# Performance work log

Hardware: AMD Instinct MI355X
Metric: run time of the kernel (lower is better)

The kernel has to match this reference:

```python
import jax, jax.numpy as jnp
import numpy as np

B, N, D = 32, 2048, 1024


def setup_inputs() -> dict:
    key = jax.random.key(0)
    k1, k2, k3, k4, k5, k6 = jax.random.split(key, 6)
    encoded = jax.random.normal(k1, (B, N, D), dtype=jnp.float32)
    decoder_state = jax.random.normal(k2, (B, D), dtype=jnp.float32)
    mask = jax.random.randint(k3, (B, N), 0, 2, dtype=jnp.int32)
    scale = 1.0 / np.sqrt(D)
    W1 = jax.random.normal(k4, (D, D), dtype=jnp.float32) * scale  # applied as x @ W1
    W2 = jax.random.normal(k5, (D, D), dtype=jnp.float32) * scale
    vt = jax.random.normal(k6, (D,), dtype=jnp.float32) * scale
    return {"encoded": encoded, "decoder_state": decoder_state, "mask": mask,
            "W1": W1, "W2": W2, "vt": vt}


def reference(encoded, decoder_state, mask, W1, W2, vt):
    temperature = 1.0
    # process_encoded: W1(encoded)  [B, N, D]
    enc = jnp.einsum('bnd,de->bne', encoded, W1)
    # W2(decoder_state)  [B, D] -> broadcast-add over N
    dec = decoder_state @ W2
    # vt(tanh(.)).squeeze(2)  -> logits [B, N]
    u = jnp.einsum('bnd,d->bn', jnp.tanh(enc + dec[:, None, :]), vt)
    # masked log-softmax with temperature over dim=1
    logits = u / temperature + jnp.log(mask.astype(u.dtype) + 1e-45)
    return jax.nn.log_softmax(logits, axis=1)
```

## Files before the change

kernel.cpp:

```cpp
#include <hip/hip_runtime.h>

typedef _Float16 half8 __attribute__((ext_vector_type(8)));
typedef __fp16   pk2   __attribute__((ext_vector_type(2)));
typedef float    f32x4 __attribute__((ext_vector_type(4)));

#define GLOBAL_AS __attribute__((address_space(1)))
#define LDS_AS    __attribute__((address_space(3)))

static constexpr int Bb = 32;
static constexpr int Nn = 2048;
static constexpr int Dd = 1024;
static constexpr int M  = Bb * Nn;

__global__ void prep_w1(const float* __restrict__ W1, _Float16* __restrict__ W1TT) {
    int g = blockIdx.x * 256 + threadIdx.x;
    int tile = g >> 9;
    int u = g & 511;
    int et = tile >> 5, kt = tile & 31;
    int q = u >> 7, e = u & 127;
    int d0 = kt * 32 + q * 8;
    int col = et * 128 + e;
    half8 h;
#pragma unroll
    for (int j = 0; j < 8; ++j)
        h[j] = (_Float16)W1[(size_t)(d0 + j) * Dd + col];
    *(half8*)(W1TT + (size_t)g * 8) = h;
}

__global__ void prep_enc(const float* __restrict__ A, _Float16* __restrict__ A_p) {
    int g = blockIdx.x * 256 + threadIdx.x;
    int tile = g >> 9;
    int v = g & 511;
    int row = v >> 2, kc = v & 3;
    const float* src = A + ((size_t)(tile >> 5) * 128 + row) * Dd
                         + (tile & 31) * 32 + kc * 8;
    f32x4 f0 = *(const f32x4*)src;
    f32x4 f1 = *(const f32x4*)(src + 4);
    half8 h;
    pk2 t;
    t = __builtin_amdgcn_cvt_pkrtz(f0.x, f0.y); h[0] = t[0]; h[1] = t[1];
    t = __builtin_amdgcn_cvt_pkrtz(f0.z, f0.w); h[2] = t[0]; h[3] = t[1];
    t = __builtin_amdgcn_cvt_pkrtz(f1.x, f1.y); h[4] = t[0]; h[5] = t[1];
    t = __builtin_amdgcn_cvt_pkrtz(f1.z, f1.w); h[6] = t[0]; h[7] = t[1];
    *(half8*)(A_p + (size_t)g * 8) = h;
}

__global__ void dec_kernel(const float* __restrict__ ds, const float* __restrict__ W2,
                           float* __restrict__ dec) {
    __shared__ float part[4][64];
    int b = blockIdx.x, ech = blockIdx.y;
    int tid = threadIdx.x;
    int e = ech * 64 + (tid & 63);
    int dc = tid >> 6;
    float acc = 0.f;
#pragma unroll 4
    for (int d = dc * 256; d < dc * 256 + 256; ++d)
        acc += ds[b * Dd + d] * W2[(size_t)d * Dd + e];
    part[dc][tid & 63] = acc;
    __syncthreads();
    if (tid < 64)
        dec[b * Dd + e] = part[0][tid] + part[1][tid] + part[2][tid] + part[3][tid];
}

__global__ __launch_bounds__(256) void gemm_fused_h(
    const _Float16* __restrict__ A_p,
    const _Float16* __restrict__ W1TT,
    const float* __restrict__ dec,
    const float* __restrict__ vt,
    float* __restrict__ u_part)
{
    __shared__ _Float16 As[2][4096];
    __shared__ _Float16 Bs[2][4096];
    __shared__ float usum[2][128];

    const int g = blockIdx.x;
    const int et = (g >> 3) & 7;
    const int mtile = (g & 7) + ((g >> 6) << 3);
    const int tid = threadIdx.x;
    const int lane = tid & 63, wid = tid >> 6;
    const int wm = wid & 1, we = wid >> 1;
    const int q = lane >> 4, l15 = lane & 15;

    f32x4 acc[4][4] = {};

    const int b = mtile >> 4;
    float vtv[4], dcv[4];
#pragma unroll
    for (int nt = 0; nt < 4; ++nt) {
        int e = et * 128 + we * 64 + nt * 16 + l15;
        vtv[nt] = vt[e];
        dcv[nt] = dec[b * Dd + e];
    }
    asm volatile("s_waitcnt vmcnt(0)" ::: "memory");

    const _Float16* abase = A_p + (size_t)mtile * 32 * 4096
                            + ((size_t)(wid * 2) * 64 + lane) * 8;
    const _Float16* bbase = W1TT + (size_t)et * 32 * 4096
                            + ((size_t)(wid * 2) * 64 + lane) * 8;
    _Float16* adst[2] = { &As[0][(wid * 2) * 64 * 8], &As[1][(wid * 2) * 64 * 8] };
    _Float16* bdst[2] = { &Bs[0][(wid * 2) * 64 * 8], &Bs[1][(wid * 2) * 64 * 8] };

    auto issue = [&](int kt) {
        const _Float16* ak = abase + (size_t)kt * 4096;
        const _Float16* bk = bbase + (size_t)kt * 4096;
        const int s = kt & 1;
        __builtin_amdgcn_global_load_lds((const GLOBAL_AS void*)ak,
                                         (LDS_AS void*)adst[s], 16, 0, 0);
        __builtin_amdgcn_global_load_lds((const GLOBAL_AS void*)(ak + 512),
                                         (LDS_AS void*)(adst[s] + 512), 16, 0, 0);
        __builtin_amdgcn_global_load_lds((const GLOBAL_AS void*)bk,
                                         (LDS_AS void*)bdst[s], 16, 0, 0);
        __builtin_amdgcn_global_load_lds((const GLOBAL_AS void*)(bk + 512),
                                         (LDS_AS void*)(bdst[s] + 512), 16, 0, 0);
    };

    issue(0);

#pragma unroll 1
    for (int kt = 0; kt < 32; ++kt) {
        const int s = kt & 1;
        if (kt < 31) {
            issue(kt + 1);
            asm volatile("s_waitcnt vmcnt(4)" ::: "memory");
        } else {
            asm volatile("s_waitcnt vmcnt(0)" ::: "memory");
        }
        asm volatile("s_barrier" ::: "memory");

        half8 af[4], bf[4];
#pragma unroll
        for (int mt = 0; mt < 4; ++mt)
            af[mt] = *(const half8*)&As[s][(wm * 64 + mt * 16 + l15) * 32 + q * 8];
#pragma unroll
        for (int nt = 0; nt < 4; ++nt)
            bf[nt] = *(const half8*)&Bs[s][(q * 128 + we * 64 + nt * 16 + l15) * 8];
#pragma unroll
        for (int mt = 0; mt < 4; ++mt)
#pragma unroll
            for (int nt = 0; nt < 4; ++nt)
                acc[mt][nt] = __builtin_amdgcn_mfma_f32_16x16x32_f16(
                    af[mt], bf[nt], acc[mt][nt], 0, 0, 0);

        asm volatile("s_waitcnt lgkmcnt(0)" ::: "memory");
        asm volatile("s_barrier" ::: "memory");
    }

#pragma unroll
    for (int mt = 0; mt < 4; ++mt) {
#pragma unroll
        for (int r = 0; r < 4; ++r) {
            float s = 0.f;
#pragma unroll
            for (int nt = 0; nt < 4; ++nt) {
                float x = acc[mt][nt][r] + dcv[nt];
                float ex = __expf(2.f * x);
                float th = 1.f - 2.f * __builtin_amdgcn_rcpf(ex + 1.f);
                s += th * vtv[nt];
            }
#pragma unroll
            for (int off = 1; off < 16; off <<= 1) s += __shfl_xor(s, off, 16);
            if (l15 == 0) usum[we][wm * 64 + mt * 16 + q * 4 + r] = s;
        }
    }
    __syncthreads();
    if (tid < 128)
        u_part[(size_t)et * M + (size_t)mtile * 128 + tid] = usum[0][tid] + usum[1][tid];
}

__global__ __launch_bounds__(256) void gemm_fused_f32(
    const float* __restrict__ A, const _Float16* __restrict__ W1TT,
    const float* __restrict__ dec, const float* __restrict__ vt,
    float* __restrict__ u_part)
{
    __shared__ _Float16 As2[4 * 128 * 8];
    __shared__ _Float16 Bs2[512 * 8];
    __shared__ float usum[2][128];

    const int et = blockIdx.x, mtile = blockIdx.y;
    const int tid = threadIdx.x;
    const int lane = tid & 63, wid = tid >> 6;
    const int wm = wid & 1, we = wid >> 1;
    const int q = lane >> 4, l15 = lane & 15;
    f32x4 acc[4][4] = {};

    const int arow = tid >> 1, khalf = tid & 1;
    const float* aptr = A + (size_t)(mtile * 128 + arow) * Dd + khalf * 16;
    const int q0 = khalf * 2;
    const _Float16* bbase = W1TT + (size_t)et * 32 * 4096
                            + ((size_t)(wid * 2) * 64 + lane) * 8;
    _Float16* bdst0 = &Bs2[(wid * 2 + 0) * 64 * 8];
    _Float16* bdst1 = &Bs2[(wid * 2 + 1) * 64 * 8];

#pragma unroll 1
    for (int kt = 0; kt < 32; ++kt) {
        const _Float16* bk = bbase + (size_t)kt * 4096;
        __builtin_amdgcn_global_load_lds((const GLOBAL_AS void*)bk,
                                         (LDS_AS void*)bdst0, 16, 0, 0);
        __builtin_amdgcn_global_load_lds((const GLOBAL_AS void*)(bk + 512),
                                         (LDS_AS void*)bdst1, 16, 0, 0);
        const float4* ap = (const float4*)(aptr + kt * 32);
        float4 f0 = ap[0], f1 = ap[1], f2 = ap[2], f3 = ap[3];
        half8 h0, h1;
        {
            pk2 t;
            t = __builtin_amdgcn_cvt_pkrtz(f0.x, f0.y); h0[0] = t[0]; h0[1] = t[1];
            t = __builtin_amdgcn_cvt_pkrtz(f0.z, f0.w); h0[2] = t[0]; h0[3] = t[1];
            t = __builtin_amdgcn_cvt_pkrtz(f1.x, f1.y); h0[4] = t[0]; h0[5] = t[1];
            t = __builtin_amdgcn_cvt_pkrtz(f1.z, f1.w); h0[6] = t[0]; h0[7] = t[1];
            t = __builtin_amdgcn_cvt_pkrtz(f2.x, f2.y); h1[0] = t[0]; h1[1] = t[1];
            t = __builtin_amdgcn_cvt_pkrtz(f2.z, f2.w); h1[2] = t[0]; h1[3] = t[1];
            t = __builtin_amdgcn_cvt_pkrtz(f3.x, f3.y); h1[4] = t[0]; h1[5] = t[1];
            t = __builtin_amdgcn_cvt_pkrtz(f3.z, f3.w); h1[6] = t[0]; h1[7] = t[1];
        }
        *(half8*)&As2[((q0 + 0) * 128 + arow) * 8] = h0;
        *(half8*)&As2[((q0 + 1) * 128 + arow) * 8] = h1;
        __syncthreads();

        half8 af[4], bf[4];
#pragma unroll
        for (int mt = 0; mt < 4; ++mt)
            af[mt] = *(const half8*)&As2[(q * 128 + wm * 64 + mt * 16 + l15) * 8];
#pragma unroll
        for (int nt = 0; nt < 4; ++nt)
            bf[nt] = *(const half8*)&Bs2[(q * 128 + we * 64 + nt * 16 + l15) * 8];
#pragma unroll
        for (int mt = 0; mt < 4; ++mt)
#pragma unroll
            for (int nt = 0; nt < 4; ++nt)
                acc[mt][nt] = __builtin_amdgcn_mfma_f32_16x16x32_f16(
                    af[mt], bf[nt], acc[mt][nt], 0, 0, 0);
        __syncthreads();
    }

    const int b = mtile >> 4;
    float vtv[4], dcv[4];
#pragma unroll
    for (int nt = 0; nt < 4; ++nt) {
        int e = et * 128 + we * 64 + nt * 16 + l15;
        vtv[nt] = vt[e];
        dcv[nt] = dec[b * Dd + e];
    }
#pragma unroll
    for (int mt = 0; mt < 4; ++mt) {
#pragma unroll
        for (int r = 0; r < 4; ++r) {
            float s = 0.f;
#pragma unroll
            for (int nt = 0; nt < 4; ++nt) {
                float x = acc[mt][nt][r] + dcv[nt];
                float ex = __expf(2.f * x);
                float th = 1.f - 2.f * __builtin_amdgcn_rcpf(ex + 1.f);
                s += th * vtv[nt];
            }
#pragma unroll
            for (int off = 1; off < 16; off <<= 1) s += __shfl_xor(s, off, 16);
            if (l15 == 0) usum[we][wm * 64 + mt * 16 + q * 4 + r] = s;
        }
    }
    __syncthreads();
    if (tid < 128)
        u_part[(size_t)et * M + (size_t)mtile * 128 + tid] = usum[0][tid] + usum[1][tid];
}

__global__ void softmax_k(const float* __restrict__ up, const int* __restrict__ mask,
                          float* __restrict__ out) {
    __shared__ float red[8];
    int b = blockIdx.x, tid = threadIdx.x;
    float l[8];
#pragma unroll
    for (int i = 0; i < 8; ++i) {
        int n = i * 256 + tid;
        float s = up[(size_t)b * Nn + n];
#pragma unroll
        for (int et = 1; et < 8; ++et) s += up[(size_t)et * M + (size_t)b * Nn + n];
        l[i] = s + (mask[b * Nn + n] ? 0.f : -103.278931f);
    }
    float m = l[0];
#pragma unroll
    for (int i = 1; i < 8; ++i) m = fmaxf(m, l[i]);
#pragma unroll
    for (int o = 32; o >= 1; o >>= 1) m = fmaxf(m, __shfl_xor(m, o, 64));
    if ((tid & 63) == 0) red[tid >> 6] = m;
    __syncthreads();
    m = fmaxf(fmaxf(red[0], red[1]), fmaxf(red[2], red[3]));
    float s = 0.f;
#pragma unroll
    for (int i = 0; i < 8; ++i) s += expf(l[i] - m);
#pragma unroll
    for (int o = 32; o >= 1; o >>= 1) s += __shfl_xor(s, o, 64);
    if ((tid & 63) == 0) red[4 + (tid >> 6)] = s;
    __syncthreads();
    float lse = m + logf(red[4] + red[5] + red[6] + red[7]);
#pragma unroll
    for (int i = 0; i < 8; ++i)
        out[(size_t)b * Nn + i * 256 + tid] = l[i] - lse;
}

extern "C" void kernel_launch(void* const* d_in, const int* in_sizes, int n_in,
                              void* d_out, int out_size, void* d_ws, size_t ws_size,
                              hipStream_t stream) {
    const float* encoded = (const float*)d_in[0];
    const float* dstate  = (const float*)d_in[1];
    const int*   mask    = (const int*)d_in[2];
    const float* W1      = (const float*)d_in[3];
    const float* W2      = (const float*)d_in[4];
    const float* vt      = (const float*)d_in[5];
    float* out = (float*)d_out;

    char* ws = (char*)d_ws;
    float*    u_part = (float*)ws;
    float*    dec    = (float*)(ws + (size_t)8 * M * 4);
    _Float16* W1TT   = (_Float16*)(ws + (size_t)8 * M * 4 + (size_t)Bb * Dd * 4);
    _Float16* A_p    = (_Float16*)(ws + (size_t)8 * M * 4 + (size_t)Bb * Dd * 4
                                   + (size_t)Dd * Dd * 2);
    const size_t needed = (size_t)8 * M * 4 + (size_t)Bb * Dd * 4
                        + (size_t)Dd * Dd * 2 + (size_t)M * Dd * 2;

    prep_w1<<<512, 256, 0, stream>>>(W1, W1TT);
    dec_kernel<<<dim3(32, 16), 256, 0, stream>>>(dstate, W2, dec);
    if (ws_size >= needed) {
        prep_enc<<<32768, 256, 0, stream>>>(encoded, A_p);
        gemm_fused_h<<<4096, 256, 0, stream>>>(A_p, W1TT, dec, vt, u_part);
    } else {
        gemm_fused_f32<<<dim3(8, 512), 256, 0, stream>>>(encoded, W1TT, dec, vt, u_part);
    }
    softmax_k<<<32, 256, 0, stream>>>(u_part, mask, out);
}
```

Measured before the change: 596.1 us.

## Replace 128x128 GEMM with 256x256-tile 8-wave kernel using swizzled LDS layout

Replaces the 128x128-tile fused GEMM with a 256x256-tile, 512-thread kernel that uses 128KB of dynamic LDS. It splits each K-step into four MFMA quadrants with staged global-to-LDS prefetches, barriers and s_setprio, and remaps workgroups across XCDs. The prep kernels now write an XOR-swizzled 64-wide K-chunk layout (prep_enc transposes through LDS) to avoid bank conflicts, and u_part drops from 8 to 4 E-partials. The goal is more data reuse per tile and better MFMA utilisation. It also removes the fp32 fallback path that ran when workspace was too small, and the big LDS footprint limits occupancy to one block per CU.

```diff
diff --git a/kernel.cpp b/kernel.cpp
--- a/kernel.cpp
+++ b/kernel.cpp
@@ -12,37 +12,52 @@
 static constexpr int Dd = 1024;
 static constexpr int M  = Bb * Nn;
 
+
 __global__ void prep_w1(const float* __restrict__ W1, _Float16* __restrict__ W1TT) {
     int g = blockIdx.x * 256 + threadIdx.x;
-    int tile = g >> 9;
-    int u = g & 511;
-    int et = tile >> 5, kt = tile & 31;
-    int q = u >> 7, e = u & 127;
-    int d0 = kt * 32 + q * 8;
-    int col = et * 128 + e;
-    half8 h;
+    int chunk = g >> 10;
+    int u = g & 1023;
+    int q = u >> 7, sc = u & 127;
+    int cl = sc ^ (2 * (q & 3));
+    int et = chunk >> 5, t = (chunk >> 1) & 15, h = chunk & 1;
+    int e  = et * 256 + h * 128 + cl;
+    int k0 = t * 64 + q * 8;
+    half8 hh;
 #pragma unroll
     for (int j = 0; j < 8; ++j)
-        h[j] = (_Float16)W1[(size_t)(d0 + j) * Dd + col];
-    *(half8*)(W1TT + (size_t)g * 8) = h;
+        hh[j] = (_Float16)W1[(size_t)(k0 + j) * Dd + e];
+    *(half8*)(W1TT + (size_t)g * 8) = hh;
 }
 
 __global__ void prep_enc(const float* __restrict__ A, _Float16* __restrict__ A_p) {
-    int g = blockIdx.x * 256 + threadIdx.x;
-    int tile = g >> 9;
-    int v = g & 511;
-    int row = v >> 2, kc = v & 3;
-    const float* src = A + ((size_t)(tile >> 5) * 128 + row) * Dd
-                         + (tile & 31) * 32 + kc * 8;
-    f32x4 f0 = *(const f32x4*)src;
-    f32x4 f1 = *(const f32x4*)(src + 4);
-    half8 h;
-    pk2 t;
-    t = __builtin_amdgcn_cvt_pkrtz(f0.x, f0.y); h[0] = t[0]; h[1] = t[1];
-    t = __builtin_amdgcn_cvt_pkrtz(f0.z, f0.w); h[2] = t[0]; h[3] = t[1];
-    t = __builtin_amdgcn_cvt_pkrtz(f1.x, f1.y); h[4] = t[0]; h[5] = t[1];
-    t = __builtin_amdgcn_cvt_pkrtz(f1.z, f1.w); h[6] = t[0]; h[7] = t[1];
-    *(half8*)(A_p + (size_t)g * 8) = h;
+    __shared__ _Float16 T[128 * 64];
+    const int c = blockIdx.x;
+    const int tid = threadIdx.x;
+    const int mtile = c >> 5, t = (c >> 1) & 15, h = c & 1;
+    const int r = tid >> 1, kh = tid & 1;
+    const float* src = A + (size_t)(mtile * 256 + h * 128 + r) * Dd + t * 64 + kh * 32;
+    const int rx = r & 7;
+#pragma unroll
+    for (int i = 0; i < 4; ++i) {
+        f32x4 a  = *(const f32x4*)(src + i * 8);
+        f32x4 b2 = *(const f32x4*)(src + i * 8 + 4);
+        half8 hh; pk2 p;
+        p = __builtin_amdgcn_cvt_pkrtz(a.x, a.y);   hh[0] = p[0]; hh[1] = p[1];
+        p = __builtin_amdgcn_cvt_pkrtz(a.z, a.w);   hh[2] = p[0]; hh[3] = p[1];
+        p = __builtin_amdgcn_cvt_pkrtz(b2.x, b2.y); hh[4] = p[0]; hh[5] = p[1];
+        p = __builtin_amdgcn_cvt_pkrtz(b2.z, b2.w); hh[6] = p[0]; hh[7] = p[1];
+        *(half8*)(T + r * 64 + (((kh * 4 + i) ^ rx) * 8)) = hh;
+    }
+    __syncthreads();
+    const size_t cb = (size_t)c * 8192;
+#pragma unroll
+    for (int i = 0; i < 4; ++i) {
+        int u = i * 256 + tid;
+        int q = u >> 7, sr = u & 127;
+        int lr = sr ^ (2 * (q & 3));
+        half8 hh = *(const half8*)(T + lr * 64 + ((q ^ (lr & 7)) * 8));
+        *(half8*)(A_p + cb + (size_t)u * 8) = hh;
+    }
 }
 
 __global__ void dec_kernel(const float* __restrict__ ds, const float* __restrict__ W2,
@@ -62,204 +77,183 @@
         dec[b * Dd + e] = part[0][tid] + part[1][tid] + part[2][tid] + part[3][tid];
 }
 
-__global__ __launch_bounds__(256) void gemm_fused_h(
-    const _Float16* __restrict__ A_p,
-    const _Float16* __restrict__ W1TT,
-    const float* __restrict__ dec,
-    const float* __restrict__ vt,
-    float* __restrict__ u_part)
-{
-    __shared__ _Float16 As[2][4096];
-    __shared__ _Float16 Bs[2][4096];
-    __shared__ float usum[2][128];
-
-    const int g = blockIdx.x;
-    const int et = (g >> 3) & 7;
-    const int mtile = (g & 7) + ((g >> 6) << 3);
-    const int tid = threadIdx.x;
-    const int lane = tid & 63, wid = tid >> 6;
-    const int wm = wid & 1, we = wid >> 1;
-    const int q = lane >> 4, l15 = lane & 15;
-
-    f32x4 acc[4][4] = {};
-
-    const int b = mtile >> 4;
-    float vtv[4], dcv[4];
-#pragma unroll
-    for (int nt = 0; nt < 4; ++nt) {
-        int e = et * 128 + we * 64 + nt * 16 + l15;
-        vtv[nt] = vt[e];
-        dcv[nt] = dec[b * Dd + e];
-    }
-    asm volatile("s_waitcnt vmcnt(0)" ::: "memory");
-
-    const _Float16* abase = A_p + (size_t)mtile * 32 * 4096
-                            + ((size_t)(wid * 2) * 64 + lane) * 8;
-    const _Float16* bbase = W1TT + (size_t)et * 32 * 4096
-                            + ((size_t)(wid * 2) * 64 + lane) * 8;
-    _Float16* adst[2] = { &As[0][(wid * 2) * 64 * 8], &As[1][(wid * 2) * 64 * 8] };
-    _Float16* bdst[2] = { &Bs[0][(wid * 2) * 64 * 8], &Bs[1][(wid * 2) * 64 * 8] };
-
-    auto issue = [&](int kt) {
-        const _Float16* ak = abase + (size_t)kt * 4096;
-        const _Float16* bk = bbase + (size_t)kt * 4096;
-        const int s = kt & 1;
-        __builtin_amdgcn_global_load_lds((const GLOBAL_AS void*)ak,
-                                         (LDS_AS void*)adst[s], 16, 0, 0);
-        __builtin_amdgcn_global_load_lds((const GLOBAL_AS void*)(ak + 512),
-                                         (LDS_AS void*)(adst[s] + 512), 16, 0, 0);
-        __builtin_amdgcn_global_load_lds((const GLOBAL_AS void*)bk,
-                                         (LDS_AS void*)bdst[s], 16, 0, 0);
-        __builtin_amdgcn_global_load_lds((const GLOBAL_AS void*)(bk + 512),
-                                         (LDS_AS void*)(bdst[s] + 512), 16, 0, 0);
-    };
-
-    issue(0);
-
-#pragma unroll 1
-    for (int kt = 0; kt < 32; ++kt) {
-        const int s = kt & 1;
-        if (kt < 31) {
-            issue(kt + 1);
-            asm volatile("s_waitcnt vmcnt(4)" ::: "memory");
-        } else {
-            asm volatile("s_waitcnt vmcnt(0)" ::: "memory");
-        }
-        asm volatile("s_barrier" ::: "memory");
-
-        half8 af[4], bf[4];
-#pragma unroll
-        for (int mt = 0; mt < 4; ++mt)
-            af[mt] = *(const half8*)&As[s][(wm * 64 + mt * 16 + l15) * 32 + q * 8];
-#pragma unroll
-        for (int nt = 0; nt < 4; ++nt)
-            bf[nt] = *(const half8*)&Bs[s][(q * 128 + we * 64 + nt * 16 + l15) * 8];
-#pragma unroll
-        for (int mt = 0; mt < 4; ++mt)
-#pragma unroll
-            for (int nt = 0; nt < 4; ++nt)
-                acc[mt][nt] = __builtin_amdgcn_mfma_f32_16x16x32_f16(
-                    af[mt], bf[nt], acc[mt][nt], 0, 0, 0);
-
-        asm volatile("s_waitcnt lgkmcnt(0)" ::: "memory");
-        asm volatile("s_barrier" ::: "memory");
-    }
-
-#pragma unroll
-    for (int mt = 0; mt < 4; ++mt) {
-#pragma unroll
-        for (int r = 0; r < 4; ++r) {
-            float s = 0.f;
-#pragma unroll
-            for (int nt = 0; nt < 4; ++nt) {
-                float x = acc[mt][nt][r] + dcv[nt];
-                float ex = __expf(2.f * x);
-                float th = 1.f - 2.f * __builtin_amdgcn_rcpf(ex + 1.f);
-                s += th * vtv[nt];
-            }
-#pragma unroll
-            for (int off = 1; off < 16; off <<= 1) s += __shfl_xor(s, off, 16);
-            if (l15 == 0) usum[we][wm * 64 + mt * 16 + q * 4 + r] = s;
-        }
-    }
-    __syncthreads();
-    if (tid < 128)
-        u_part[(size_t)et * M + (size_t)mtile * 128 + tid] = usum[0][tid] + usum[1][tid];
-}
-
-__global__ __launch_bounds__(256) void gemm_fused_f32(
-    const float* __restrict__ A, const _Float16* __restrict__ W1TT,
+__global__ __launch_bounds__(512) void gemm8(
+    const _Float16* __restrict__ A_p, const _Float16* __restrict__ W1TT,
     const float* __restrict__ dec, const float* __restrict__ vt,
     float* __restrict__ u_part)
 {
-    __shared__ _Float16 As2[4 * 128 * 8];
-    __shared__ _Float16 Bs2[512 * 8];
-    __shared__ float usum[2][128];
-
-    const int et = blockIdx.x, mtile = blockIdx.y;
-    const int tid = threadIdx.x;
+    extern __shared__ _Float16 lds[];
+
+    const int g  = blockIdx.x;
+    const int wg = (g & 7) * 128 + (g >> 3);
+    const int et    = wg & 3;
+    const int mtile = wg >> 2;
+
+    const int tid  = threadIdx.x;
     const int lane = tid & 63, wid = tid >> 6;
-    const int wm = wid & 1, we = wid >> 1;
-    const int q = lane >> 4, l15 = lane & 15;
-    f32x4 acc[4][4] = {};
-
-    const int arow = tid >> 1, khalf = tid & 1;
-    const float* aptr = A + (size_t)(mtile * 128 + arow) * Dd + khalf * 16;
-    const int q0 = khalf * 2;
-    const _Float16* bbase = W1TT + (size_t)et * 32 * 4096
-                            + ((size_t)(wid * 2) * 64 + lane) * 8;
-    _Float16* bdst0 = &Bs2[(wid * 2 + 0) * 64 * 8];
-    _Float16* bdst1 = &Bs2[(wid * 2 + 1) * 64 * 8];
+    const int wr = wid >> 2, wc = wid & 3;
+    const int qq = lane >> 4, l15 = lane & 15;
+    const int l15s = l15 ^ (2 * qq);
+    const int rA = wr * 16 + l15s;
+    const int rB = wc * 16 + l15s;
+
+    f32x4 acc[8][4] = {};
+
+    const int b = mtile >> 3;
+    float vtv[4], dcv[4];
+#pragma unroll
+    for (int nf = 0; nf < 4; ++nf) {
+        int e = et * 256 + (nf >> 1) * 128 + (nf & 1) * 64 + wc * 16 + l15;
+        vtv[nf] = vt[e];
+        dcv[nf] = dec[b * Dd + e];
+    }
+    asm volatile("s_waitcnt vmcnt(0)" ::: "memory");
+
+    const size_t abase = (size_t)mtile * 32 * 8192;
+    const size_t bbase = (size_t)et * 32 * 8192;
+    const int uoff = tid * 8;
+
+    auto stA = [&](int t2, int h) {
+        const _Float16* gp = A_p + abase + ((size_t)(t2 * 2 + h) << 13) + uoff;
+        _Float16* lp = lds + ((((t2 & 1) * 2 + h) << 13) + (wid << 9));
+        __builtin_amdgcn_global_load_lds((const GLOBAL_AS void*)gp,
+                                         (LDS_AS void*)lp, 16, 0, 0);
+        __builtin_amdgcn_global_load_lds((const GLOBAL_AS void*)(gp + 4096),
+                                         (LDS_AS void*)(lp + 4096), 16, 0, 0);
+    };
+    auto stB = [&](int t2, int h) {
+        const _Float16* gp = W1TT + bbase + ((size_t)(t2 * 2 + h) << 13) + uoff;
+        _Float16* lp = lds + (32768 + (((t2 & 1) * 2 + h) << 13) + (wid << 9));
+        __builtin_amdgcn_global_load_lds((const GLOBAL_AS void*)gp,
+                                         (LDS_AS void*)lp, 16, 0, 0);
+        __builtin_amdgcn_global_load_lds((const GLOBAL_AS void*)(gp + 4096),
+                                         (LDS_AS void*)(lp + 4096), 16, 0, 0);
+    };
+
+    stA(0, 0); stB(0, 0); stB(0, 1); stA(0, 1); stA(1, 0); stB(1, 0); stB(1, 1);
+    asm volatile("s_waitcnt vmcnt(10)" ::: "memory");
+    asm volatile("s_barrier" ::: "memory");
+
+    half8 af[4][2], bf0[2][2], bf1[2][2];
 
 #pragma unroll 1
-    for (int kt = 0; kt < 32; ++kt) {
-        const _Float16* bk = bbase + (size_t)kt * 4096;
-        __builtin_amdgcn_global_load_lds((const GLOBAL_AS void*)bk,
-                                         (LDS_AS void*)bdst0, 16, 0, 0);
-        __builtin_amdgcn_global_load_lds((const GLOBAL_AS void*)(bk + 512),
-                                         (LDS_AS void*)bdst1, 16, 0, 0);
-        const float4* ap = (const float4*)(aptr + kt * 32);
-        float4 f0 = ap[0], f1 = ap[1], f2 = ap[2], f3 = ap[3];
-        half8 h0, h1;
-        {
-            pk2 t;
-            t = __builtin_amdgcn_cvt_pkrtz(f0.x, f0.y); h0[0] = t[0]; h0[1] = t[1];
-            t = __builtin_amdgcn_cvt_pkrtz(f0.z, f0.w); h0[2] = t[0]; h0[3] = t[1];
-            t = __builtin_amdgcn_cvt_pkrtz(f1.x, f1.y); h0[4] = t[0]; h0[5] = t[1];
-            t = __builtin_amdgcn_cvt_pkrtz(f1.z, f1.w); h0[6] = t[0]; h0[7] = t[1];
-            t = __builtin_amdgcn_cvt_pkrtz(f2.x, f2.y); h1[0] = t[0]; h1[1] = t[1];
-            t = __builtin_amdgcn_cvt_pkrtz(f2.z, f2.w); h1[2] = t[0]; h1[3] = t[1];
-            t = __builtin_amdgcn_cvt_pkrtz(f3.x, f3.y); h1[4] = t[0]; h1[5] = t[1];
-            t = __builtin_amdgcn_cvt_pkrtz(f3.z, f3.w); h1[6] = t[0]; h1[7] = t[1];
+    for (int t = 0; t < 16; ++t) {
+        const int Ab0 = (t & 1) * 16384;
+        const int Ab1 = Ab0 + 8192;
+        const int Bb0 = 32768 + Ab0;
+        const int Bb1 = Bb0 + 8192;
+
+#pragma unroll
+        for (int ks = 0; ks < 2; ++ks) {
+            const int qb = ((ks * 4 + qq) * 128) * 8;
+#pragma unroll
+            for (int m = 0; m < 4; ++m)
+                af[m][ks] = *(const half8*)&lds[Ab0 + qb + (m * 32 + rA) * 8];
+#pragma unroll
+            for (int j = 0; j < 2; ++j)
+                bf0[j][ks] = *(const half8*)&lds[Bb0 + qb + (j * 64 + rB) * 8];
         }
-        *(half8*)&As2[((q0 + 0) * 128 + arow) * 8] = h0;
-        *(half8*)&As2[((q0 + 1) * 128 + arow) * 8] = h1;
-        __syncthreads();
-
-        half8 af[4], bf[4];
-#pragma unroll
-        for (int mt = 0; mt < 4; ++mt)
-            af[mt] = *(const half8*)&As2[(q * 128 + wm * 64 + mt * 16 + l15) * 8];
-#pragma unroll
-        for (int nt = 0; nt < 4; ++nt)
-            bf[nt] = *(const half8*)&Bs2[(q * 128 + we * 64 + nt * 16 + l15) * 8];
-#pragma unroll
-        for (int mt = 0; mt < 4; ++mt)
-#pragma unroll
-            for (int nt = 0; nt < 4; ++nt)
-                acc[mt][nt] = __builtin_amdgcn_mfma_f32_16x16x32_f16(
-                    af[mt], bf[nt], acc[mt][nt], 0, 0, 0);
-        __syncthreads();
-    }
-
-    const int b = mtile >> 4;
-    float vtv[4], dcv[4];
-#pragma unroll
-    for (int nt = 0; nt < 4; ++nt) {
-        int e = et * 128 + we * 64 + nt * 16 + l15;
-        vtv[nt] = vt[e];
-        dcv[nt] = dec[b * Dd + e];
-    }
-#pragma unroll
-    for (int mt = 0; mt < 4; ++mt) {
+        if (t < 15) stA(t + 1, 1);
+        if (t < 15) asm volatile("s_waitcnt vmcnt(10)" ::: "memory");
+        else        asm volatile("s_waitcnt vmcnt(2)"  ::: "memory");
+        asm volatile("s_barrier" ::: "memory");
+        asm volatile("s_waitcnt lgkmcnt(0)" ::: "memory");
+        __builtin_amdgcn_s_setprio(1);
+#pragma unroll
+        for (int m = 0; m < 4; ++m)
+#pragma unroll
+            for (int j = 0; j < 2; ++j) {
+                acc[m][j] = __builtin_amdgcn_mfma_f32_16x16x32_f16(af[m][0], bf0[j][0], acc[m][j], 0, 0, 0);
+                acc[m][j] = __builtin_amdgcn_mfma_f32_16x16x32_f16(af[m][1], bf0[j][1], acc[m][j], 0, 0, 0);
+            }
+        __builtin_amdgcn_s_setprio(0);
+        asm volatile("s_barrier" ::: "memory");
+
+#pragma unroll
+        for (int ks = 0; ks < 2; ++ks) {
+            const int qb = ((ks * 4 + qq) * 128) * 8;
+#pragma unroll
+            for (int j = 0; j < 2; ++j)
+                bf1[j][ks] = *(const half8*)&lds[Bb1 + qb + (j * 64 + rB) * 8];
+        }
+        if (t < 14) stA(t + 2, 0);
+        if (t < 14)       asm volatile("s_waitcnt vmcnt(10)" ::: "memory");
+        else if (t == 14) asm volatile("s_waitcnt vmcnt(8)"  ::: "memory");
+        else              asm volatile("s_waitcnt vmcnt(0)"  ::: "memory");
+        asm volatile("s_barrier" ::: "memory");
+        asm volatile("s_waitcnt lgkmcnt(0)" ::: "memory");
+        __builtin_amdgcn_s_setprio(1);
+#pragma unroll
+        for (int m = 0; m < 4; ++m)
+#pragma unroll
+            for (int j = 0; j < 2; ++j) {
+                acc[m][2 + j] = __builtin_amdgcn_mfma_f32_16x16x32_f16(af[m][0], bf1[j][0], acc[m][2 + j], 0, 0, 0);
+                acc[m][2 + j] = __builtin_amdgcn_mfma_f32_16x16x32_f16(af[m][1], bf1[j][1], acc[m][2 + j], 0, 0, 0);
+            }
+        __builtin_amdgcn_s_setprio(0);
+        asm volatile("s_barrier" ::: "memory");
+
+#pragma unroll
+        for (int ks = 0; ks < 2; ++ks) {
+            const int qb = ((ks * 4 + qq) * 128) * 8;
+#pragma unroll
+            for (int m = 0; m < 4; ++m)
+                af[m][ks] = *(const half8*)&lds[Ab1 + qb + (m * 32 + rA) * 8];
+        }
+        if (t < 14) stB(t + 2, 0);
+        asm volatile("s_barrier" ::: "memory");
+        asm volatile("s_waitcnt lgkmcnt(0)" ::: "memory");
+        __builtin_amdgcn_s_setprio(1);
+#pragma unroll
+        for (int m = 0; m < 4; ++m)
+#pragma unroll
+            for (int j = 0; j < 2; ++j) {
+                acc[4 + m][j] = __builtin_amdgcn_mfma_f32_16x16x32_f16(af[m][0], bf0[j][0], acc[4 + m][j], 0, 0, 0);
+                acc[4 + m][j] = __builtin_amdgcn_mfma_f32_16x16x32_f16(af[m][1], bf0[j][1], acc[4 + m][j], 0, 0, 0);
+            }
+        __builtin_amdgcn_s_setprio(0);
+        asm volatile("s_barrier" ::: "memory");
+
+        if (t < 14) stB(t + 2, 1);
+        if (t < 14)       asm volatile("s_waitcnt vmcnt(10)" ::: "memory");
+        else if (t == 14) asm volatile("s_waitcnt vmcnt(4)"  ::: "memory");
+        asm volatile("s_barrier" ::: "memory");
+        __builtin_amdgcn_s_setprio(1);
+#pragma unroll
+        for (int m = 0; m < 4; ++m)
+#pragma unroll
+            for (int j = 0; j < 2; ++j) {
+                acc[4 + m][2 + j] = __builtin_amdgcn_mfma_f32_16x16x32_f16(af[m][0], bf1[j][0], acc[4 + m][2 + j], 0, 0, 0);
+                acc[4 + m][2 + j] = __builtin_amdgcn_mfma_f32_16x16x32_f16(af[m][1], bf1[j][1], acc[4 + m][2 + j], 0, 0, 0);
+            }
+        __builtin_amdgcn_s_setprio(0);
+        asm volatile("s_barrier" ::: "memory");
+    }
+
+    float* usum = (float*)lds;
+#pragma unroll
+    for (int hm = 0; hm < 8; ++hm) {
+        const int h = hm >> 2, m = hm & 3;
 #pragma unroll
         for (int r = 0; r < 4; ++r) {
             float s = 0.f;
 #pragma unroll
-            for (int nt = 0; nt < 4; ++nt) {
-                float x = acc[mt][nt][r] + dcv[nt];
+            for (int nf = 0; nf < 4; ++nf) {
+                float x  = acc[hm][nf][r] + dcv[nf];
                 float ex = __expf(2.f * x);
-                float th = 1.f - 2.f * __builtin_amdgcn_rcpf(ex + 1.f);
-                s += th * vtv[nt];
+                s += (1.f - 2.f * __builtin_amdgcn_rcpf(ex + 1.f)) * vtv[nf];
             }
 #pragma unroll
             for (int off = 1; off < 16; off <<= 1) s += __shfl_xor(s, off, 16);
-            if (l15 == 0) usum[we][wm * 64 + mt * 16 + q * 4 + r] = s;
+            if (l15 == 0)
+                usum[wc * 256 + h * 128 + m * 32 + wr * 16 + qq * 4 + r] = s;
         }
     }
     __syncthreads();
-    if (tid < 128)
-        u_part[(size_t)et * M + (size_t)mtile * 128 + tid] = usum[0][tid] + usum[1][tid];
+    if (tid < 256) {
+        float v = usum[tid] + usum[256 + tid] + usum[512 + tid] + usum[768 + tid];
+        u_part[(size_t)et * M + (size_t)mtile * 256 + tid] = v;
+    }
 }
 
 __global__ void softmax_k(const float* __restrict__ up, const int* __restrict__ mask,
@@ -272,7 +266,7 @@
         int n = i * 256 + tid;
         float s = up[(size_t)b * Nn + n];
 #pragma unroll
-        for (int et = 1; et < 8; ++et) s += up[(size_t)et * M + (size_t)b * Nn + n];
+        for (int et = 1; et < 4; ++et) s += up[(size_t)et * M + (size_t)b * Nn + n];
         l[i] = s + (mask[b * Nn + n] ? 0.f : -103.278931f);
     }
     float m = l[0];
@@ -309,20 +303,21 @@
 
     char* ws = (char*)d_ws;
     float*    u_part = (float*)ws;
-    float*    dec    = (float*)(ws + (size_t)8 * M * 4);
-    _Float16* W1TT   = (_Float16*)(ws + (size_t)8 * M * 4 + (size_t)Bb * Dd * 4);
-    _Float16* A_p    = (_Float16*)(ws + (size_t)8 * M * 4 + (size_t)Bb * Dd * 4
+    float*    dec    = (float*)(ws + (size_t)4 * M * 4);
+    _Float16* W1TT   = (_Float16*)(ws + (size_t)4 * M * 4 + (size_t)Bb * Dd * 4);
+    _Float16* A_p    = (_Float16*)(ws + (size_t)4 * M * 4 + (size_t)Bb * Dd * 4
                                    + (size_t)Dd * Dd * 2);
-    const size_t needed = (size_t)8 * M * 4 + (size_t)Bb * Dd * 4
-                        + (size_t)Dd * Dd * 2 + (size_t)M * Dd * 2;
+
+    static bool attr_done = false;
+    if (!attr_done) {
+        hipFuncSetAttribute(reinterpret_cast<const void*>(gemm8),
+                            hipFuncAttributeMaxDynamicSharedMemorySize, 131072);
+        attr_done = true;
+    }
 
     prep_w1<<<512, 256, 0, stream>>>(W1, W1TT);
     dec_kernel<<<dim3(32, 16), 256, 0, stream>>>(dstate, W2, dec);
-    if (ws_size >= needed) {
-        prep_enc<<<32768, 256, 0, stream>>>(encoded, A_p);
-        gemm_fused_h<<<4096, 256, 0, stream>>>(A_p, W1TT, dec, vt, u_part);
-    } else {
-        gemm_fused_f32<<<dim3(8, 512), 256, 0, stream>>>(encoded, W1TT, dec, vt, u_part);
-    }
+    prep_enc<<<8192, 256, 0, stream>>>(encoded, A_p);
+    gemm8<<<1024, 512, 131072, stream>>>(A_p, W1TT, dec, vt, u_part);
     softmax_k<<<32, 256, 0, stream>>>(u_part, mask, out);
 }
```

Result: faster. 569.7 us (-4.4%).
